# Performance work log

Hardware: AMD Instinct MI355X
Metric: run time of the kernel (lower is better)

Reference implementation:

```python
import jax, jax.numpy as jnp
from jax import lax
import numpy as np

NH = 8   # num_heads
WS = 7   # windowsize
SR = 2   # sr_ratio


def _conv(x, w, b, stride=1, padding=0, groups=1):
    y = lax.conv_general_dilated(x, w, (stride, stride), [(padding, padding)] * 2,
                                 dimension_numbers=('NCHW', 'OIHW', 'NCHW'),
                                 feature_group_count=groups)
    return y + b[None, :, None, None]


def _ln(x, g, b, eps=1e-5):
    m = x.mean(-1, keepdims=True)
    v = ((x - m) ** 2).mean(-1, keepdims=True)
    return (x - m) * lax.rsqrt(v + eps) * g + b


def _local_branch(q_, kv_img, dilation, stride, fc_w, sh_w, lc_w, lc_b, scale, H, W):
    # q_: [B,NH,N,hd]; kv_img: [B,C,H,W] with C = NH*hd
    B, C = kv_img.shape[0], kv_img.shape[1]
    hd = q_.shape[-1]
    pad_b = (-H) % stride
    pad_r = (-W) % stride
    kv = jnp.pad(kv_img, ((0, 0), (0, 0), (0, pad_b), (0, pad_r)), mode='reflect')
    nH, nW = (H + pad_b) // stride, (W + pad_r) // stride
    L = nH * nW
    # nn.Unfold(kernel=WS, stride, dilation): effective kernel == stride, so
    # windows tile exactly; sample each stride x stride tile at step `dilation`.
    kv = kv.reshape(B, C, nH, stride, nW, stride)[:, :, :, ::dilation, :, ::dilation]  # [B,C,nH,WS,nW,WS]
    kv = kv.transpose(0, 1, 3, 5, 2, 4).reshape(B, NH, hd, WS * WS, L)
    kv = kv.transpose(0, 1, 3, 4, 2).reshape(B, NH, WS * WS, L * hd)
    # AdaptiveAvgPool2d((None, hd)) on last dim of size L*hd -> hd buckets of L
    kv = kv.reshape(B, NH, WS * WS, hd, L).mean(-1)
    kv = (kv @ fc_w) @ sh_w                                  # [B,NH,49,2*hd]
    k_, v_ = kv[..., :hd], kv[..., hd:]
    attn = jax.nn.softmax(jnp.einsum('bhnd,bhkd->bhnk', q_, k_) * scale, axis=-1)
    v_img = v_.transpose(0, 1, 3, 2).reshape(B, C, WS, WS)
    v_ = v_ + _conv(v_img, lc_w, lc_b, padding=1, groups=C).reshape(B, NH, hd, WS * WS).transpose(0, 1, 3, 2)
    out = jnp.einsum('bhnk,bhkd->bhnd', attn, v_)            # [B,NH,N,hd]
    return out.transpose(0, 2, 1, 3).reshape(B, -1, C)


def setup_inputs() -> dict:
    key = jax.random.key(0)
    ks = jax.random.split(key, 24)
    B, H, W, dim = 2, 112, 112, 512
    N = H * W
    d0, d1, hd = 64, 224, 28
    dl = dim - d0  # 448

    def w(k, shape):
        return jax.random.normal(k, shape, jnp.float32) * 0.02

    return dict(
        x=jax.random.normal(ks[0], (B, N, dim), jnp.float32),
        Wq=w(ks[1], (dim, dim)),
        Wkv_g=w(ks[2], (d0, 2 * d0)),
        sr_w=w(ks[3], (d0, d0, SR, SR)), sr_b=w(ks[4], (d0,)),
        ln_g=jnp.ones((d0,), jnp.float32), ln_b=jnp.zeros((d0,), jnp.float32),
        lcg_w=w(ks[5], (d0, 1, 3, 3)), lcg_b=w(ks[6], (d0,)),
        kvl_dw=w(ks[7], (dl, 1, 3, 3)), kvl_db=w(ks[8], (dl,)),
        kvl_pw=w(ks[9], (dl, dl, 1, 1)), kvl_pb=w(ks[10], (dl,)),
        fc1_w=w(ks[11], (hd, hd)), sh1_w=w(ks[12], (hd, 2 * hd)),
        lc1_w=w(ks[13], (d1, 1, 3, 3)), lc1_b=w(ks[14], (d1,)),
        fc2_w=w(ks[15], (hd, hd)), sh2_w=w(ks[16], (hd, 2 * hd)),
        lc2_w=w(ks[17], (d1, 1, 3, 3)), lc2_b=w(ks[18], (d1,)),
        proj_w=w(ks[19], (dim, dim)), proj_b=w(ks[20], (dim,)),
        H=H, W=W,
    )


def reference(x, Wq, Wkv_g, sr_w, sr_b, ln_g, ln_b, lcg_w, lcg_b, kvl_dw, kvl_db,
              kvl_pw, kvl_pb, fc1_w, sh1_w, lc1_w, lc1_b, fc2_w, sh2_w, lc2_w, lc2_b,
              proj_w, proj_b, H, W):
    B, N, C = x.shape
    d0 = 64
    dl = C - d0        # 448
    hd = 224 // NH     # 28
    q = x @ Wq
    # ---- global spatially-reduced branch (1 head, dim 64) ----
    q_g = q[:, :, :d0]                                      # [B,N,64]
    x_g = x[:, :, :d0].transpose(0, 2, 1).reshape(B, d0, H, W)
    x_g = _conv(x_g, sr_w, sr_b, stride=SR)                 # [B,64,H/2,W/2]
    Hs, Ws_ = H // SR, W // SR
    Nr = Hs * Ws_
    x_g = _ln(x_g.reshape(B, d0, Nr).transpose(0, 2, 1), ln_g, ln_b)
    kvg = x_g @ Wkv_g
    k_g, v_g = kvg[..., :d0], kvg[..., d0:]
    attn_g = jax.nn.softmax(jnp.einsum('bnd,bmd->bnm', q_g, k_g) * d0 ** -0.5, axis=-1)
    v_img = v_g.transpose(0, 2, 1).reshape(B, d0, Hs, Ws_)
    v_g = v_g + _conv(v_img, lcg_w, lcg_b, padding=1, groups=d0).reshape(B, d0, Nr).transpose(0, 2, 1)
    out_g = jnp.einsum('bnm,bmd->bnd', attn_g, v_g)         # [B,N,64]
    # ---- local windowed branches (8 heads, dim 224 each) ----
    q_l = q[:, :, d0:].reshape(B, N, NH, -1).transpose(0, 2, 1, 3)  # [B,NH,N,56]
    x_l = x[:, :, d0:].reshape(B, H, W, dl).transpose(0, 3, 1, 2)
    kv_l = _conv(_conv(x_l, kvl_dw, kvl_db, padding=1, groups=dl), kvl_pw, kvl_pb)
    scale = hd ** -0.5
    out1 = _local_branch(q_l[:, :, :, :hd], kv_l[:, :224], 1, WS,
                         fc1_w, sh1_w, lc1_w, lc1_b, scale, H, W)
    out2 = _local_branch(q_l[:, :, :, hd:], kv_l[:, 224:], SR, SR * (WS - 1) + 1,
                         fc2_w, sh2_w, lc2_w, lc2_b, scale, H, W)
    return jnp.concatenate([out_g, out1, out2], -1) @ proj_w + proj_b
```

## Files before the change

kernel.cpp:

```cpp
#include <hip/hip_runtime.h>
#include <hip/hip_bf16.h>
#include <math.h>
#include <stdint.h>

static constexpr int B_    = 2;
static constexpr int N_    = 12544;
static constexpr int DIM_  = 512;
static constexpr int D0_   = 64;
static constexpr int DL_   = 448;
static constexpr int Himg  = 112;
static constexpr int Wimg  = 112;
static constexpr int HS_   = 56;
static constexpr int NR_   = 3136;
static constexpr int NH_   = 8;
static constexpr int HD_   = 28;
static constexpr int NSPLIT = 4;

typedef unsigned short ushort_t;
typedef __attribute__((ext_vector_type(8))) short short8_t;
typedef __attribute__((ext_vector_type(4))) float float4v;
typedef __attribute__((ext_vector_type(4))) unsigned uint4v;
typedef __attribute__((ext_vector_type(2))) unsigned uint2v;

static __device__ inline ushort_t bf16r(float x) {
    unsigned u = __builtin_bit_cast(unsigned, x);
    u = (u + 0x7FFFu + ((u >> 16) & 1u)) >> 16;
    return (ushort_t)u;
}
static __device__ inline float bf16tof(ushort_t h) {
    unsigned u = ((unsigned)h) << 16;
    return __builtin_bit_cast(float, u);
}
static __device__ inline unsigned pack_bf16(float lo, float hi) {
    unsigned a = __builtin_bit_cast(unsigned, lo);
    unsigned b = __builtin_bit_cast(unsigned, hi);
    a = (a + 0x7FFFu + ((a >> 16) & 1u)) >> 16;
    b = (b + 0x7FFFu + ((b >> 16) & 1u)) >> 16;
    return a | (b << 16);
}
static __device__ inline unsigned cvtpk(float lo, float hi) {
    float2 f2; f2.x = lo; f2.y = hi;
    __hip_bfloat162 h = __float22bfloat162_rn(f2);
    unsigned u;
    __builtin_memcpy(&u, &h, 4);
    return u;
}

using gptr_t = const __attribute__((address_space(1))) void*;
using lptr_t = __attribute__((address_space(3))) void*;
static __device__ inline void gload16(const void* g, void* l) {
    __builtin_amdgcn_global_load_lds((gptr_t)(uintptr_t)g, (lptr_t)(uintptr_t)l, 16, 0, 0);
}

template<bool HASBIAS, bool OUT16>
__global__ __launch_bounds__(256, 2)
void gemm_bf16_kernel(const ushort_t* __restrict__ A,
                      const ushort_t* __restrict__ Bt,
                      const float* __restrict__ bias,
                      void* __restrict__ Cv,
                      int Nn, int K, int ldc) {
    constexpr int BM = 128, BK = 64;
    __shared__ __align__(16) ushort_t As[BM * BK];
    __shared__ __align__(16) ushort_t Bs[BM * BK];
    const int bm = blockIdx.x * BM;
    const int bn = blockIdx.y * BM;
    const int tid = threadIdx.x;
    const int l15 = tid & 15;
    const int g   = (tid & 63) >> 4;
    const int w   = tid >> 6;
    const int wr  = w >> 1, wc = w & 1;

    float4v acc[4][4];
    #pragma unroll
    for (int m = 0; m < 4; ++m)
        #pragma unroll
        for (int n = 0; n < 4; ++n) acc[m][n] = (float4v){0.f, 0.f, 0.f, 0.f};

    for (int k0 = 0; k0 < K; k0 += BK) {
        #pragma unroll
        for (int i = 0; i < 4; ++i) {
            int c = i * 256 + tid;
            int r = c >> 3, ch = c & 7;
            int sch = ch ^ (r & 7);
            gload16(A  + (size_t)(bm + r) * K + k0 + sch * 8, (void*)(As + c * 8));
            gload16(Bt + (size_t)(bn + r) * K + k0 + sch * 8, (void*)(Bs + c * 8));
        }
        __syncthreads();

        short8_t af[4][2], bfr[4][2];
        #pragma unroll
        for (int m = 0; m < 4; ++m) {
            int ar = wr * 64 + m * 16 + l15;
            #pragma unroll
            for (int h = 0; h < 2; ++h)
                af[m][h] = *(const short8_t*)((const char*)As + ar * 128 + (((h * 4 + g) ^ (ar & 7)) * 16));
        }
        #pragma unroll
        for (int n = 0; n < 4; ++n) {
            int br = wc * 64 + n * 16 + l15;
            #pragma unroll
            for (int h = 0; h < 2; ++h)
                bfr[n][h] = *(const short8_t*)((const char*)Bs + br * 128 + (((h * 4 + g) ^ (br & 7)) * 16));
        }
        #pragma unroll
        for (int m = 0; m < 4; ++m)
            #pragma unroll
            for (int n = 0; n < 4; ++n) {
                acc[m][n] = __builtin_amdgcn_mfma_f32_16x16x32_bf16(af[m][0], bfr[n][0], acc[m][n], 0, 0, 0);
                acc[m][n] = __builtin_amdgcn_mfma_f32_16x16x32_bf16(af[m][1], bfr[n][1], acc[m][n], 0, 0, 0);
            }
        __syncthreads();
    }

    #pragma unroll
    for (int n = 0; n < 4; ++n) {
        int ccol = bn + wc * 64 + n * 16 + l15;
        if (ccol < Nn) {
            float bv = HASBIAS ? bias[ccol] : 0.f;
            #pragma unroll
            for (int m = 0; m < 4; ++m) {
                int crow = bm + wr * 64 + m * 16 + g * 4;
                #pragma unroll
                for (int j = 0; j < 4; ++j) {
                    float v = acc[m][n][j] + bv;
                    if (OUT16)
                        ((ushort_t*)Cv)[(size_t)(crow + j) * ldc + ccol] = bf16r(v);
                    else
                        ((float*)Cv)[(size_t)(crow + j) * ldc + ccol] = v;
                }
            }
        }
    }
}

__global__ __launch_bounds__(256)
void prep_kernel(const float* __restrict__ Wq, const float* __restrict__ kvl_pw,
                 const float* __restrict__ proj_w, const float* __restrict__ sr_w,
                 const float* __restrict__ x,
                 ushort_t* __restrict__ wqt, ushort_t* __restrict__ pwt,
                 ushort_t* __restrict__ projt, float* __restrict__ srwt,
                 ushort_t* __restrict__ xbf) {
    int idx = blockIdx.x * 256 + threadIdx.x;
    if (idx < 262144) {
        int n = idx >> 9, k = idx & 511;
        wqt[idx] = bf16r(Wq[(size_t)k * 512 + n]);
    } else if (idx < 491520) {
        int i = idx - 262144;
        int n = i / 448, k = i % 448;
        float v = (n < 448) ? kvl_pw[(size_t)n * 448 + k] : 0.f;
        pwt[i] = bf16r(v);
    } else if (idx < 753664) {
        int i = idx - 491520;
        int n = i >> 9, k = i & 511;
        projt[i] = bf16r(proj_w[(size_t)k * 512 + n]);
    } else if (idx < 770048) {
        int i = idx - 753664;
        int f = i >> 6, o2 = i & 63;
        srwt[i] = sr_w[o2 * 256 + f];
    } else {
        int i = idx - 770048;
        const float4v* p = (const float4v*)(x + (size_t)i * 8);
        float4v a = p[0], b = p[1];
        uint4v u;
        u[0] = pack_bf16(a[0], a[1]);
        u[1] = pack_bf16(a[2], a[3]);
        u[2] = pack_bf16(b[0], b[1]);
        u[3] = pack_bf16(b[2], b[3]);
        *(uint4v*)(xbf + (size_t)i * 8) = u;
    }
}

__global__ __launch_bounds__(256, 2)
void fused3_kernel(const ushort_t* __restrict__ xbf, const ushort_t* __restrict__ wqt,
                   ushort_t* __restrict__ q16,
                   const float* __restrict__ kvl_dw, const float* __restrict__ kvl_db,
                   ushort_t* __restrict__ dwtb,
                   const float* __restrict__ x, const float* __restrict__ srwt,
                   const float* __restrict__ sr_b, const float* __restrict__ ln_g,
                   const float* __restrict__ ln_b, const float* __restrict__ wkv,
                   ushort_t* __restrict__ kgb, float* __restrict__ vg) {
    const int bid = blockIdx.x;
    const int tid = threadIdx.x;
    __shared__ __align__(16) char smem[32768];

    if (bid < 784) {
        ushort_t* As = (ushort_t*)smem;
        ushort_t* Bs = (ushort_t*)(smem + 16384);
        const int bm = (bid % 196) * 128;
        const int bn = (bid / 196) * 128;
        const int l15 = tid & 15;
        const int g   = (tid & 63) >> 4;
        const int w   = tid >> 6;
        const int wr  = w >> 1, wc = w & 1;
        float4v acc[4][4];
        #pragma unroll
        for (int m = 0; m < 4; ++m)
            #pragma unroll
            for (int n = 0; n < 4; ++n) acc[m][n] = (float4v){0.f, 0.f, 0.f, 0.f};
        for (int k0 = 0; k0 < 512; k0 += 64) {
            #pragma unroll
            for (int i = 0; i < 4; ++i) {
                int c = i * 256 + tid;
                int r = c >> 3, ch = c & 7;
                int sch = ch ^ (r & 7);
                gload16(xbf + (size_t)(bm + r) * 512 + k0 + sch * 8, (void*)(As + c * 8));
                gload16(wqt + (size_t)(bn + r) * 512 + k0 + sch * 8, (void*)(Bs + c * 8));
            }
            __syncthreads();
            short8_t af[4][2], bfr[4][2];
            #pragma unroll
            for (int m = 0; m < 4; ++m) {
                int ar = wr * 64 + m * 16 + l15;
                #pragma unroll
                for (int h = 0; h < 2; ++h)
                    af[m][h] = *(const short8_t*)((const char*)As + ar * 128 + (((h * 4 + g) ^ (ar & 7)) * 16));
            }
            #pragma unroll
            for (int n = 0; n < 4; ++n) {
                int br = wc * 64 + n * 16 + l15;
                #pragma unroll
                for (int h = 0; h < 2; ++h)
                    bfr[n][h] = *(const short8_t*)((const char*)Bs + br * 128 + (((h * 4 + g) ^ (br & 7)) * 16));
            }
            #pragma unroll
            for (int m = 0; m < 4; ++m)
                #pragma unroll
                for (int n = 0; n < 4; ++n) {
                    acc[m][n] = __builtin_amdgcn_mfma_f32_16x16x32_bf16(af[m][0], bfr[n][0], acc[m][n], 0, 0, 0);
                    acc[m][n] = __builtin_amdgcn_mfma_f32_16x16x32_bf16(af[m][1], bfr[n][1], acc[m][n], 0, 0, 0);
                }
            __syncthreads();
        }
        #pragma unroll
        for (int n = 0; n < 4; ++n) {
            int ccol = bn + wc * 64 + n * 16 + l15;
            #pragma unroll
            for (int m = 0; m < 4; ++m) {
                int crow = bm + wr * 64 + m * 16 + g * 4;
                #pragma unroll
                for (int j = 0; j < 4; ++j)
                    q16[(size_t)(crow + j) * 512 + ccol] = bf16r(acc[m][n][j]);
            }
        }
    } else if (bid < 3528) {
        int idx = (bid - 784) * 256 + tid;
        int c4 = idx % 112;
        int t1 = idx / 112;
        int xx = t1 % 112;
        int t2 = t1 / 112;
        int yg = t2 % 28;
        int b  = t2 / 28;
        int c0 = c4 * 4;
        int y0 = yg * 4;
        float4v w4[9];
        #pragma unroll
        for (int kt = 0; kt < 9; ++kt) {
            w4[kt][0] = kvl_dw[(c0 + 0) * 9 + kt];
            w4[kt][1] = kvl_dw[(c0 + 1) * 9 + kt];
            w4[kt][2] = kvl_dw[(c0 + 2) * 9 + kt];
            w4[kt][3] = kvl_dw[(c0 + 3) * 9 + kt];
        }
        float4v bv = *(const float4v*)(kvl_db + c0);
        float4v acc[4];
        #pragma unroll
        for (int o2 = 0; o2 < 4; ++o2) acc[o2] = bv;
        #pragma unroll
        for (int yy = 0; yy < 6; ++yy) {
            int Y = y0 - 1 + yy;
            if (Y < 0 || Y >= Himg) continue;
            #pragma unroll
            for (int xt = 0; xt < 3; ++xt) {
                int X = xx - 1 + xt;
                if (X < 0 || X >= Wimg) continue;
                uint2v q2 = *(const uint2v*)(xbf + ((size_t)b * N_ + Y * Wimg + X) * DIM_ + D0_ + c0);
                float4v v;
                v[0] = bf16tof((ushort_t)(q2[0] & 0xffffu));
                v[1] = bf16tof((ushort_t)(q2[0] >> 16));
                v[2] = bf16tof((ushort_t)(q2[1] & 0xffffu));
                v[3] = bf16tof((ushort_t)(q2[1] >> 16));
                constexpr int olo_t[6] = {0, 0, 0, 1, 2, 3};
                constexpr int ohi_t[6] = {0, 1, 2, 3, 3, 3};
                #pragma unroll
                for (int o2 = olo_t[yy]; o2 <= ohi_t[yy]; ++o2) {
                    float4v wv = w4[(yy - o2) * 3 + xt];
                    acc[o2][0] += v[0] * wv[0];
                    acc[o2][1] += v[1] * wv[1];
                    acc[o2][2] += v[2] * wv[2];
                    acc[o2][3] += v[3] * wv[3];
                }
            }
        }
        #pragma unroll
        for (int o2 = 0; o2 < 4; ++o2) {
            uint2v pk;
            pk[0] = pack_bf16(acc[o2][0], acc[o2][1]);
            pk[1] = pack_bf16(acc[o2][2], acc[o2][3]);
            *(uint2v*)(dwtb + ((size_t)b * N_ + (y0 + o2) * Wimg + xx) * DL_ + c0) = pk;
        }
    } else {
        float* xs    = (float*)smem;
        float* lnv_s = (float*)(smem + 4096);
        const int blk4 = bid - 3528;
        const int grp  = tid >> 6;
        const int o    = tid & 63;
        const int pos  = blk4 * 4 + grp;
        const int b = pos / NR_, n = pos % NR_;
        const int y = n / HS_, xx = n % HS_;
        #pragma unroll
        for (int tap = 0; tap < 4; ++tap) {
            int ky = tap / 2, kx = tap % 2;
            xs[grp * 256 + tap * 64 + o] =
                x[((size_t)b * N_ + (2 * y + ky) * Wimg + 2 * xx + kx) * DIM_ + o];
        }
        __syncthreads();
        float sum = sr_b[o];
        for (int i = 0; i < 64; ++i) {
            const float* wr = srwt + (i * 4) * 64 + o;
            sum += xs[grp * 256 + 0 * 64 + i] * wr[0] + xs[grp * 256 + 1 * 64 + i] * wr[64]
                 + xs[grp * 256 + 2 * 64 + i] * wr[128] + xs[grp * 256 + 3 * 64 + i] * wr[192];
        }
        float m = sum;
        #pragma unroll
        for (int off = 1; off < 64; off <<= 1) m += __shfl_xor(m, off);
        m *= (1.0f / 64.0f);
        float d = sum - m;
        float v = d * d;
        #pragma unroll
        for (int off = 1; off < 64; off <<= 1) v += __shfl_xor(v, off);
        v *= (1.0f / 64.0f);
        float lnv = d * rsqrtf(v + 1e-5f) * ln_g[o] + ln_b[o];
        lnv_s[grp * 64 + o] = lnv;
        __syncthreads();
        float s0 = 0.f, s1 = 0.f;
        for (int i = 0; i < 64; ++i) {
            float lv = lnv_s[grp * 64 + i];
            s0 += lv * wkv[i * 128 + o];
            s1 += lv * wkv[i * 128 + o + 64];
        }
        const float SCK = 0.125f * 1.44269504088896340736f;
        kgb[((size_t)b * NR_ + n) * 64 + o] = bf16r(s0 * SCK);
        vg[((size_t)b * NR_ + n) * 64 + o] = s1;
    }
}

__global__ __launch_bounds__(256, 2)
void fused2_kernel(const ushort_t* __restrict__ dwtb, const ushort_t* __restrict__ pwt,
                   const float* __restrict__ kvl_pb, ushort_t* __restrict__ kvl16,
                   const float* __restrict__ vg, const float* __restrict__ lcg_w,
                   const float* __restrict__ lcg_b, ushort_t* __restrict__ vtb) {
    const int bid = blockIdx.x;
    const int tid = threadIdx.x;
    __shared__ __align__(16) char smem[32768];

    if (bid < 784) {
        ushort_t* As = (ushort_t*)smem;
        ushort_t* Bs = (ushort_t*)(smem + 16384);
        const int bm = (bid % 196) * 128;
        const int bn = (bid / 196) * 128;
        const int l15 = tid & 15;
        const int g   = (tid & 63) >> 4;
        const int w   = tid >> 6;
        const int wr  = w >> 1, wc = w & 1;
        float4v acc[4][4];
        #pragma unroll
        for (int m = 0; m < 4; ++m)
            #pragma unroll
            for (int n = 0; n < 4; ++n) acc[m][n] = (float4v){0.f, 0.f, 0.f, 0.f};
        for (int k0 = 0; k0 < 448; k0 += 64) {
            #pragma unroll
            for (int i = 0; i < 4; ++i) {
                int c = i * 256 + tid;
                int r = c >> 3, ch = c & 7;
                int sch = ch ^ (r & 7);
                gload16(dwtb + (size_t)(bm + r) * 448 + k0 + sch * 8, (void*)(As + c * 8));
                gload16(pwt  + (size_t)(bn + r) * 448 + k0 + sch * 8, (void*)(Bs + c * 8));
            }
            __syncthreads();
            short8_t af[4][2], bfr[4][2];
            #pragma unroll
            for (int m = 0; m < 4; ++m) {
                int ar = wr * 64 + m * 16 + l15;
                #pragma unroll
                for (int h = 0; h < 2; ++h)
                    af[m][h] = *(const short8_t*)((const char*)As + ar * 128 + (((h * 4 + g) ^ (ar & 7)) * 16));
            }
            #pragma unroll
            for (int n = 0; n < 4; ++n) {
                int br = wc * 64 + n * 16 + l15;
                #pragma unroll
                for (int h = 0; h < 2; ++h)
                    bfr[n][h] = *(const short8_t*)((const char*)Bs + br * 128 + (((h * 4 + g) ^ (br & 7)) * 16));
            }
            #pragma unroll
            for (int m = 0; m < 4; ++m)
                #pragma unroll
                for (int n = 0; n < 4; ++n) {
                    acc[m][n] = __builtin_amdgcn_mfma_f32_16x16x32_bf16(af[m][0], bfr[n][0], acc[m][n], 0, 0, 0);
                    acc[m][n] = __builtin_amdgcn_mfma_f32_16x16x32_bf16(af[m][1], bfr[n][1], acc[m][n], 0, 0, 0);
                }
            __syncthreads();
        }
        #pragma unroll
        for (int n = 0; n < 4; ++n) {
            int ccol = bn + wc * 64 + n * 16 + l15;
            if (ccol < 448) {
                float bv = kvl_pb[ccol];
                #pragma unroll
                for (int m = 0; m < 4; ++m) {
                    int crow = bm + wr * 64 + m * 16 + g * 4;
                    #pragma unroll
                    for (int j = 0; j < 4; ++j)
                        kvl16[(size_t)(crow + j) * 448 + ccol] = bf16r(acc[m][n][j] + bv);
                }
            }
        }
    } else {
        float* ld = (float*)smem;
        const int lb = bid - 784;
        const int b = lb / 49, n0 = (lb % 49) * 64;
        #pragma unroll
        for (int i = 0; i < 16; ++i) {
            int idx = i * 256 + tid;
            int n = idx >> 6, c = idx & 63;
            int nn = n0 + n;
            int y = nn / HS_, xx = nn % HS_;
            float sum = vg[((size_t)b * NR_ + nn) * 64 + c] + lcg_b[c];
            #pragma unroll
            for (int ky = 0; ky < 3; ++ky)
                #pragma unroll
                for (int kx = 0; kx < 3; ++kx) {
                    int yy = y + ky - 1, x2 = xx + kx - 1;
                    if (yy >= 0 && yy < HS_ && x2 >= 0 && x2 < HS_)
                        sum += vg[((size_t)b * NR_ + yy * HS_ + x2) * 64 + c] * lcg_w[c * 9 + ky * 3 + kx];
                }
            ld[n * 65 + c] = sum;
        }
        __syncthreads();
        #pragma unroll
        for (int i = 0; i < 16; ++i) {
            int idx = i * 256 + tid;
            int d = idx >> 6, nn = idx & 63;
            vtb[(size_t)(b * 64 + d) * NR_ + n0 + nn] = bf16r(ld[nn * 65 + d]);
        }
    }
}

template<int L, int NBW, int STRIDE, int DIL, int CHOFF>
__device__ inline void lm_body(int blk, int t, float* slo, float* shi,
                               const ushort_t* __restrict__ kvl16,
                               float* __restrict__ kvm) {
    const int n = blk % 49;
    const int h = (blk / 49) % NH_;
    const int b = blk / (49 * NH_);
    const int wy = n / 7, wx = n % 7;

    if (t < L) {
        const int by = t / NBW, bx = t % NBW;
        int Y = by * STRIDE + DIL * wy;
        int X = bx * STRIDE + DIL * wx;
        if (Y >= Himg) Y = 2 * Himg - 2 - Y;
        if (X >= Wimg) X = 2 * Wimg - 2 - X;
        const ushort_t* src = kvl16 + ((size_t)b * N_ + Y * Wimg + X) * DL_ + CHOFF + h * HD_;
        float v[28];
        #pragma unroll
        for (int i = 0; i < 7; ++i) {
            uint2v q2 = ((const uint2v*)src)[i];
            v[i * 4]     = bf16tof((ushort_t)(q2[0] & 0xffffu));
            v[i * 4 + 1] = bf16tof((ushort_t)(q2[0] >> 16));
            v[i * 4 + 2] = bf16tof((ushort_t)(q2[1] & 0xffffu));
            v[i * 4 + 3] = bf16tof((ushort_t)(q2[1] >> 16));
        }
        const int f0 = t * HD_;
        const int bin0 = f0 / L;
        const int nlo = min(HD_, (bin0 + 1) * L - f0);
        float s0 = 0.f, s1 = 0.f;
        #pragma unroll
        for (int j = 0; j < HD_; ++j) {
            if (j < nlo) s0 += v[j]; else s1 += v[j];
        }
        slo[t] = s0;
        shi[t] = s1;
    }
    __syncthreads();
    if (t < HD_) {
        const int t_lo = (t * L) / HD_;
        const int t_hi = min(L - 1, (t * L + L - 1) / HD_);
        float sum = 0.f;
        for (int u = t_lo; u <= t_hi; ++u) {
            int f0 = u * HD_;
            int b0 = f0 / L;
            int b1 = (f0 + HD_ - 1) / L;
            if (b0 == t) sum += slo[u];
            if (b1 == t && b1 != b0) sum += shi[u];
        }
        kvm[(size_t)blk * HD_ + t] = sum * (1.0f / (float)L);
    }
}

__global__ __launch_bounds__(512)
void fused_ag_lm_kernel(const ushort_t* __restrict__ q16,
                        const ushort_t* __restrict__ kgb,
                        const ushort_t* __restrict__ vtb,
                        ushort_t* __restrict__ osp16, float* __restrict__ mls,
                        const ushort_t* __restrict__ kvl16,
                        float* __restrict__ kvm1, float* __restrict__ kvm2) {
    const int bid = blockIdx.x;
    const int tid = threadIdx.x;
    __shared__ __align__(16) char smem[32768];
    ushort_t* Ks = (ushort_t*)smem;
    ushort_t* Vs = (ushort_t*)(smem + 16384);

    if (bid >= 784) {
        float* slo = (float*)smem;
        float* shi = (float*)(smem + 1024);
        int lmid = bid - 784;
        int blk = lmid % 784;
        if (lmid < 784) lm_body<256, 16, 7, 1, 0>(blk, tid, slo, shi, kvl16, kvm1);
        else            lm_body<81, 9, 13, 2, 224>(blk, tid, slo, shi, kvl16, kvm2);
        return;
    }

    const int split = (bid / 98) & 3;
    const int b     = (bid / 98) >> 2;
    const int q0    = (bid % 98) * 128;
    const int w     = tid >> 6;
    const int l     = tid & 63;
    const int l15   = l & 15;
    const int g     = l >> 4;
    const int lx    = l15 & 7;

    short8_t qf[2];
    {
        const ushort_t* qrow = q16 + ((size_t)b * N_ + q0 + w * 16 + l15) * DIM_;
        qf[0] = *(const short8_t*)(qrow + g * 8);
        qf[1] = *(const short8_t*)(qrow + g * 8 + 32);
    }

    float4v o[4];
    #pragma unroll
    for (int i = 0; i < 4; ++i) o[i] = (float4v){0.f, 0.f, 0.f, 0.f};
    float m_run = -3.0e38f, l_run = 0.f;

    const int stg_r   = tid >> 3;
    const int stg_sch = (tid & 7) ^ (stg_r & 7);
    const int stg_pr  = (stg_r & 32) | (((stg_r >> 2) & 3) << 3) | (((stg_r >> 4) & 1) << 2) | (stg_r & 3);
    auto stage = [&](int t, int buf) {
        const int k0 = t * 64;
        gload16(kgb + ((size_t)(b * NR_ + k0 + stg_pr) << 6) + stg_sch * 8,
                (void*)(Ks + buf * 4096 + tid * 8));
        gload16(vtb + (size_t)(b * 64 + stg_r) * NR_ + k0 + stg_sch * 8,
                (void*)(Vs + buf * 4096 + tid * 8));
    };

    auto compute = [&](const ushort_t* Kb, const ushort_t* Vb) {
        float4v sc[4];
        #pragma unroll
        for (int c = 0; c < 4; ++c) {
            float4v acc = (float4v){0.f, 0.f, 0.f, 0.f};
            #pragma unroll
            for (int dc = 0; dc < 2; ++dc) {
                int row = c * 16 + l15;
                short8_t ak = *(const short8_t*)((const char*)Kb + row * 128 + (((g + 4 * dc) ^ lx) * 16));
                acc = __builtin_amdgcn_mfma_f32_16x16x32_bf16(ak, qf[dc], acc, 0, 0, 0);
            }
            sc[c] = acc;
        }

        float tmax = fmaxf(fmaxf(fmaxf(sc[0][0], sc[0][1]), fmaxf(sc[0][2], sc[0][3])),
                           fmaxf(fmaxf(sc[1][0], sc[1][1]), fmaxf(sc[1][2], sc[1][3])));
        tmax = fmaxf(tmax, fmaxf(fmaxf(fmaxf(sc[2][0], sc[2][1]), fmaxf(sc[2][2], sc[2][3])),
                                 fmaxf(fmaxf(sc[3][0], sc[3][1]), fmaxf(sc[3][2], sc[3][3]))));

        if (__any(tmax > m_run + 11.0f)) {
            float rmax = fmaxf(tmax, __shfl_xor(tmax, 16));
            rmax = fmaxf(rmax, __shfl_xor(rmax, 32));
            float m_new = fmaxf(m_run, rmax);
            float corr = __builtin_amdgcn_exp2f(m_run - m_new);
            float co[4];
            #pragma unroll
            for (int r = 0; r < 4; ++r) co[r] = __shfl(corr, g * 4 + r);
            #pragma unroll
            for (int dc = 0; dc < 4; ++dc)
                #pragma unroll
                for (int r = 0; r < 4; ++r) o[dc][r] *= co[r];
            l_run *= corr;
            m_run = m_new;
        }

        float p[4][4];
        float ladd = 0.f;
        #pragma unroll
        for (int c = 0; c < 4; ++c)
            #pragma unroll
            for (int r = 0; r < 4; ++r) {
                float pe = __builtin_amdgcn_exp2f(sc[c][r] - m_run);
                p[c][r] = pe;
                ladd += pe;
            }
        l_run += ladd;

        #pragma unroll
        for (int kkc = 0; kkc < 2; ++kkc) {
            uint4v au;
            au[0] = cvtpk(p[2 * kkc][0],     p[2 * kkc][1]);
            au[1] = cvtpk(p[2 * kkc][2],     p[2 * kkc][3]);
            au[2] = cvtpk(p[2 * kkc + 1][0], p[2 * kkc + 1][1]);
            au[3] = cvtpk(p[2 * kkc + 1][2], p[2 * kkc + 1][3]);
            short8_t ap = __builtin_bit_cast(short8_t, au);
            #pragma unroll
            for (int dc = 0; dc < 4; ++dc) {
                int vrow = dc * 16 + l15;
                short8_t bv = *(const short8_t*)((const char*)Vb + vrow * 128 + (((kkc * 4 + g) ^ lx) * 16));
                o[dc] = __builtin_amdgcn_mfma_f32_16x16x32_bf16(ap, bv, o[dc], 0, 0, 0);
            }
        }
    };

    const int t0 = (split * 49) / 4;
    const int t1 = ((split + 1) * 49) / 4;
    int t = t0;
    for (; t + 1 < t1; t += 2) {
        stage(t, 0);
        stage(t + 1, 1);
        __syncthreads();
        compute(Ks, Vs);
        compute(Ks + 4096, Vs + 4096);
        __syncthreads();
    }
    if (t < t1) {
        stage(t, 0);
        __syncthreads();
        compute(Ks, Vs);
    }

    float l_tot = l_run;
    l_tot += __shfl_xor(l_tot, 16);
    l_tot += __shfl_xor(l_tot, 32);

    const size_t rbase = (size_t)(split * B_ + b) * N_;
    #pragma unroll
    for (int dc = 0; dc < 4; ++dc)
        #pragma unroll
        for (int r = 0; r < 4; ++r) {
            int row = q0 + w * 16 + g * 4 + r;
            osp16[(rbase + row) * 64 + dc * 16 + l15] = bf16r(o[dc][r]);
        }
    if (l < 16) {
        int row = q0 + w * 16 + l15;
        mls[(rbase + row) * 2]     = m_run;
        mls[(rbase + row) * 2 + 1] = l_tot;
    }
}

__global__ __launch_bounds__(256)
void fcsh_vconv_kernel(const float* __restrict__ kvm1, const float* __restrict__ fc1w,
                       const float* __restrict__ sh1w, float* __restrict__ kv1,
                       const float* __restrict__ kvm2, const float* __restrict__ fc2w,
                       const float* __restrict__ sh2w, float* __restrict__ kv2,
                       const float* __restrict__ lc1w, const float* __restrict__ lc1b,
                       float* __restrict__ v1c,
                       const float* __restrict__ lc2w, const float* __restrict__ lc2b,
                       float* __restrict__ v2c) {
    int bh2 = blockIdx.x;
    const int branch = (bh2 >= 16);
    const float* kvm = branch ? kvm2 : kvm1;
    const float* fcw = branch ? fc2w : fc1w;
    const float* shw = branch ? sh2w : sh1w;
    const float* lcw = branch ? lc2w : lc1w;
    const float* lcb = branch ? lc2b : lc1b;
    float* kvout     = branch ? kv2 : kv1;
    float* vcout     = branch ? v2c : v1c;
    int bh = branch ? bh2 - 16 : bh2;
    const int h = bh % NH_;
    __shared__ float kin[49][28];
    __shared__ float tmp[49][28];
    __shared__ float fw[28 * 28];
    __shared__ float sw[28 * 56];
    __shared__ float outs[49][56];
    int t = threadIdx.x;
    for (int i = t; i < 49 * 28; i += 256) kin[i / 28][i % 28] = kvm[bh * 49 * 28 + i];
    for (int i = t; i < 28 * 28; i += 256) fw[i] = fcw[i];
    for (int i = t; i < 28 * 56; i += 256) sw[i] = shw[i];
    __syncthreads();
    for (int i = t; i < 49 * 28; i += 256) {
        int rr = i / 28, j = i % 28;
        float s = 0.f;
        for (int k = 0; k < 28; ++k) s += kin[rr][k] * fw[k * 28 + j];
        tmp[rr][j] = s;
    }
    __syncthreads();
    for (int i = t; i < 49 * 56; i += 256) {
        int rr = i / 56, j = i % 56;
        float s = 0.f;
        for (int k = 0; k < 28; ++k) s += tmp[rr][k] * sw[k * 56 + j];
        outs[rr][j] = s;
        kvout[bh * 49 * 56 + i] = s;
    }
    __syncthreads();
    for (int i = t; i < 49 * 28; i += 256) {
        int d = i % 28, n = i / 28;
        int y = n / 7, xx = n % 7;
        int c = h * HD_ + d;
        float sum = outs[n][28 + d] + lcb[c];
        #pragma unroll
        for (int ky = 0; ky < 3; ++ky)
            #pragma unroll
            for (int kx = 0; kx < 3; ++kx) {
                int yy = y + ky - 1, x2 = xx + kx - 1;
                if (yy >= 0 && yy < 7 && x2 >= 0 && x2 < 7)
                    sum += outs[yy * 7 + x2][28 + d] * lcw[c * 9 + ky * 3 + kx];
            }
        vcout[bh * 49 * 28 + i] = sum;
    }
}

__global__ __launch_bounds__(256)
void fused_local_comb_kernel(const ushort_t* __restrict__ q16,
                             const float* __restrict__ kv1, const float* __restrict__ v1c,
                             const float* __restrict__ kv2, const float* __restrict__ v2c,
                             const ushort_t* __restrict__ osp16, const float* __restrict__ mls,
                             ushort_t* __restrict__ catb) {
    const int bid = blockIdx.x;
    const int tid = threadIdx.x;
    __shared__ __align__(16) ushort_t Ks[64 * 32];
    __shared__ __align__(16) ushort_t Vt[32 * 64];

    if (bid >= 6272) {
        int idx = (bid - 6272) * 256 + tid;
        int col = idx & 63;
        size_t rn = (size_t)(idx >> 6);
        const size_t BN = (size_t)B_ * N_;
        float ms[NSPLIT], ls[NSPLIT];
        float m = -3.0e38f;
        #pragma unroll
        for (int s = 0; s < NSPLIT; ++s) {
            ms[s] = mls[(s * BN + rn) * 2];
            ls[s] = mls[(s * BN + rn) * 2 + 1];
            m = fmaxf(m, ms[s]);
        }
        float lsum = 0.f, acc = 0.f;
        #pragma unroll
        for (int s = 0; s < NSPLIT; ++s) {
            float wgt = __builtin_amdgcn_exp2f(ms[s] - m);
            lsum += ls[s] * wgt;
            acc  += bf16tof(osp16[(s * BN + rn) * 64 + col]) * wgt;
        }
        catb[rn * DIM_ + col] = bf16r(acc / lsum);
        return;
    }

    const int ybh    = bid / 196;
    const int branch = ybh & 1;
    const int bh     = ybh >> 1;
    const int b      = bh >> 3, h = bh & 7;
    const int q0     = (bid % 196) * 64;
    const int w      = tid >> 6;
    const int l      = tid & 63;
    const int l15    = l & 15;
    const int g      = l >> 4;
    const float SC2K = 0.1889822365046136f * 1.44269504088896340736f;

    const float* kvsh = branch ? kv2 : kv1;
    const float* vc   = branch ? v2c : v1c;
    const int qoff    = D0_ + h * 56 + branch * 28;
    const int outoff  = (branch ? D0_ + 224 : D0_) + h * HD_;

    {
        int row = tid >> 2, lc = tid & 3;
        int pr = (row & 32) | (((row >> 2) & 3) << 3) | (((row >> 4) & 1) << 2) | (row & 3);
        uint4v u = (uint4v){0u, 0u, 0u, 0u};
        if (pr < 49) {
            const float* src = kvsh + (bh * 49 + pr) * 56 + lc * 8;
            float vv[8];
            #pragma unroll
            for (int j2 = 0; j2 < 8; ++j2)
                vv[j2] = (lc * 8 + j2 < 28) ? src[j2] * SC2K : 0.f;
            u[0] = cvtpk(vv[0], vv[1]);
            u[1] = cvtpk(vv[2], vv[3]);
            u[2] = cvtpk(vv[4], vv[5]);
            u[3] = cvtpk(vv[6], vv[7]);
        }
        *(uint4v*)(Ks + row * 32 + (lc ^ (row & 3)) * 8) = u;
    }
    {
        int row = tid >> 3, lc = tid & 7;
        uint4v u = (uint4v){0u, 0u, 0u, 0u};
        if (row < 28) {
            float vv[8];
            #pragma unroll
            for (int j2 = 0; j2 < 8; ++j2) {
                int kc = lc * 8 + j2;
                vv[j2] = (kc < 49) ? vc[(bh * 49 + kc) * 28 + row] : 0.f;
            }
            u[0] = cvtpk(vv[0], vv[1]);
            u[1] = cvtpk(vv[2], vv[3]);
            u[2] = cvtpk(vv[4], vv[5]);
            u[3] = cvtpk(vv[6], vv[7]);
        }
        *(uint4v*)(Vt + row * 64 + (lc ^ (row & 7)) * 8) = u;
    }
    short8_t qf;
    {
        const ushort_t* qp = q16 + ((size_t)b * N_ + q0 + w * 16 + l15) * DIM_ + qoff + g * 8;
        uint2v a01 = *(const uint2v*)qp;
        uint2v a23 = (g < 3) ? *(const uint2v*)(qp + 4) : (uint2v){0u, 0u};
        uint4v uv;
        uv[0] = a01[0]; uv[1] = a01[1]; uv[2] = a23[0]; uv[3] = a23[1];
        qf = __builtin_bit_cast(short8_t, uv);
    }
    __syncthreads();

    float4v sc4[4];
    #pragma unroll
    for (int c = 0; c < 4; ++c) {
        int row = c * 16 + l15;
        short8_t ak = *(const short8_t*)(Ks + row * 32 + ((g ^ (row & 3)) * 8));
        float4v acc = (float4v){0.f, 0.f, 0.f, 0.f};
        sc4[c] = __builtin_amdgcn_mfma_f32_16x16x32_bf16(ak, qf, acc, 0, 0, 0);
    }

    float tmax = fmaxf(fmaxf(fmaxf(sc4[0][0], sc4[0][1]), fmaxf(sc4[0][2], sc4[0][3])),
                       fmaxf(fmaxf(sc4[1][0], sc4[1][1]), fmaxf(sc4[1][2], sc4[1][3])));
    tmax = fmaxf(tmax, fmaxf(fmaxf(fmaxf(sc4[2][0], sc4[2][1]), fmaxf(sc4[2][2], sc4[2][3])),
                             fmaxf(fmaxf(sc4[3][0], sc4[3][1]), fmaxf(sc4[3][2], sc4[3][3]))));
    tmax = fmaxf(tmax, __shfl_xor(tmax, 16));
    tmax = fmaxf(tmax, __shfl_xor(tmax, 32));

    float p[4][4];
    float lsum = 0.f;
    #pragma unroll
    for (int c = 0; c < 4; ++c)
        #pragma unroll
        for (int r = 0; r < 4; ++r) {
            float pe = __builtin_amdgcn_exp2f(sc4[c][r] - tmax);
            if (c >= 2 && (8 * g + 4 * (c & 1) + r) >= 17) pe = 0.f;
            p[c][r] = pe;
            lsum += pe;
        }
    lsum += __shfl_xor(lsum, 16);
    lsum += __shfl_xor(lsum, 32);
    float inv = 1.0f / lsum;

    float4v o2[2];
    o2[0] = (float4v){0.f, 0.f, 0.f, 0.f};
    o2[1] = (float4v){0.f, 0.f, 0.f, 0.f};
    #pragma unroll
    for (int kkc = 0; kkc < 2; ++kkc) {
        uint4v au;
        au[0] = cvtpk(p[2 * kkc][0],     p[2 * kkc][1]);
        au[1] = cvtpk(p[2 * kkc][2],     p[2 * kkc][3]);
        au[2] = cvtpk(p[2 * kkc + 1][0], p[2 * kkc + 1][1]);
        au[3] = cvtpk(p[2 * kkc + 1][2], p[2 * kkc + 1][3]);
        short8_t ap = __builtin_bit_cast(short8_t, au);
        #pragma unroll
        for (int dc = 0; dc < 2; ++dc) {
            int vrow = dc * 16 + l15;
            short8_t bv = *(const short8_t*)(Vt + vrow * 64 + (((kkc * 4 + g) ^ (vrow & 7)) * 8));
            o2[dc] = __builtin_amdgcn_mfma_f32_16x16x32_bf16(ap, bv, o2[dc], 0, 0, 0);
        }
    }

    float irow[4];
    #pragma unroll
    for (int r = 0; r < 4; ++r) irow[r] = __shfl(inv, g * 4 + r);
    #pragma unroll
    for (int dc = 0; dc < 2; ++dc) {
        int d = dc * 16 + l15;
        if (d < 28) {
            #pragma unroll
            for (int r = 0; r < 4; ++r) {
                int row = q0 + w * 16 + g * 4 + r;
                catb[((size_t)b * N_ + row) * DIM_ + outoff + d] = bf16r(o2[dc][r] * irow[r]);
            }
        }
    }
}

extern "C" void kernel_launch(void* const* d_in, const int* in_sizes, int n_in,
                              void* d_out, int out_size, void* d_ws, size_t ws_size,
                              hipStream_t stream) {
    const float* x      = (const float*)d_in[0];
    const float* Wq     = (const float*)d_in[1];
    const float* Wkv_g  = (const float*)d_in[2];
    const float* sr_w   = (const float*)d_in[3];
    const float* sr_b   = (const float*)d_in[4];
    const float* ln_g   = (const float*)d_in[5];
    const float* ln_b   = (const float*)d_in[6];
    const float* lcg_w  = (const float*)d_in[7];
    const float* lcg_b  = (const float*)d_in[8];
    const float* kvl_dw = (const float*)d_in[9];
    const float* kvl_db = (const float*)d_in[10];
    const float* kvl_pw = (const float*)d_in[11];
    const float* kvl_pb = (const float*)d_in[12];
    const float* fc1_w  = (const float*)d_in[13];
    const float* sh1_w  = (const float*)d_in[14];
    const float* lc1_w  = (const float*)d_in[15];
    const float* lc1_b  = (const float*)d_in[16];
    const float* fc2_w  = (const float*)d_in[17];
    const float* sh2_w  = (const float*)d_in[18];
    const float* lc2_w  = (const float*)d_in[19];
    const float* lc2_b  = (const float*)d_in[20];
    const float* proj_w = (const float*)d_in[21];
    const float* proj_b = (const float*)d_in[22];
    float* out = (float*)d_out;
    char* base = (char*)d_ws;

    size_t o = 0;
    auto alloc = [&](size_t bytes) -> void* {
        void* p = base + o;
        o = (o + bytes + 255) & ~(size_t)255;
        return p;
    };
    ushort_t* q16   = (ushort_t*)alloc((size_t)B_ * N_ * DIM_ * 2);
    ushort_t* kvl16 = (ushort_t*)alloc((size_t)B_ * N_ * DL_ * 2);
    ushort_t* osp16 = (ushort_t*)alloc((size_t)NSPLIT * B_ * N_ * 64 * 2);
    float*    mls   = (float*)   alloc((size_t)NSPLIT * B_ * N_ * 2 * 4);
    ushort_t* xcat  = (ushort_t*)alloc((size_t)B_ * N_ * DIM_ * 2);
    ushort_t* dwtb  = (ushort_t*)alloc((size_t)B_ * N_ * DL_ * 2);
    ushort_t* kgb   = (ushort_t*)alloc((size_t)B_ * NR_ * 64 * 2);
    float*    vg    = (float*)   alloc((size_t)B_ * NR_ * 64 * 4);
    ushort_t* vtb   = (ushort_t*)alloc((size_t)B_ * 64 * NR_ * 2);
    ushort_t* wqt   = (ushort_t*)alloc((size_t)512 * 512 * 2);
    ushort_t* pwt   = (ushort_t*)alloc((size_t)512 * 448 * 2);
    ushort_t* projt = (ushort_t*)alloc((size_t)512 * 512 * 2);
    float*    srwt  = (float*)   alloc((size_t)256 * 64 * 4);
    float*    kvm1  = (float*)   alloc((size_t)B_ * NH_ * 49 * HD_ * 4);
    float*    kvm2  = (float*)   alloc((size_t)B_ * NH_ * 49 * HD_ * 4);
    float*    kv1   = (float*)   alloc((size_t)B_ * NH_ * 49 * 56 * 4);
    float*    kv2   = (float*)   alloc((size_t)B_ * NH_ * 49 * 56 * 4);
    float*    v1c   = (float*)   alloc((size_t)B_ * NH_ * 49 * HD_ * 4);
    float*    v2c   = (float*)   alloc((size_t)B_ * NH_ * 49 * HD_ * 4);
    ushort_t* xbf   = xcat;
    ushort_t* catb  = xcat;

    const int M = B_ * N_;

    prep_kernel<<<9280, 256, 0, stream>>>(Wq, kvl_pw, proj_w, sr_w, x,
                                          wqt, pwt, projt, srwt, xbf);

    fused3_kernel<<<5096, 256, 0, stream>>>(xbf, wqt, q16,
                                            kvl_dw, kvl_db, dwtb,
                                            x, srwt, sr_b, ln_g, ln_b, Wkv_g,
                                            kgb, vg);

    fused2_kernel<<<882, 256, 0, stream>>>(dwtb, pwt, kvl_pb, kvl16,
                                           vg, lcg_w, lcg_b, vtb);

    fused_ag_lm_kernel<<<2352, 512, 0, stream>>>(q16, kgb, vtb, osp16, mls,
                                                 kvl16, kvm1, kvm2);

    fcsh_vconv_kernel<<<32, 256, 0, stream>>>(kvm1, fc1_w, sh1_w, kv1,
                                              kvm2, fc2_w, sh2_w, kv2,
                                              lc1_w, lc1_b, v1c,
                                              lc2_w, lc2_b, v2c);

    fused_local_comb_kernel<<<12544, 256, 0, stream>>>(q16, kv1, v1c, kv2, v2c,
                                                       osp16, mls, catb);

    gemm_bf16_kernel<true, false><<<dim3(M / 128, 4), 256, 0, stream>>>(
        catb, projt, proj_b, out, 512, 512, 512);
}
```

Before: 250.4 us.

## Move depthwise conv into prep kernel and merge both GEMMs into one launch

The depthwise 3x3 conv now runs inside the prep kernel and reads fp32 x directly instead of the bf16 copy. That lets the pointwise GEMM (dwtb x pwt) run in the same launch as the Q GEMM and the sr/LN/kv blocks, with one shared block-dispatch path. The local-conv and transpose of vg moves to its own small kernel. The goal is to rebalance work across launches and put the two large GEMMs in one grid for better occupancy. In exchange, the depthwise conv now sits in the bandwidth-bound prep kernel, and it reads fp32 x, which doubles the bytes loaded for that step.

```diff
diff --git a/kernel.cpp b/kernel.cpp
--- a/kernel.cpp
+++ b/kernel.cpp
@@ -137,9 +137,10 @@
 void prep_kernel(const float* __restrict__ Wq, const float* __restrict__ kvl_pw,
                  const float* __restrict__ proj_w, const float* __restrict__ sr_w,
                  const float* __restrict__ x,
+                 const float* __restrict__ kvl_dw, const float* __restrict__ kvl_db,
                  ushort_t* __restrict__ wqt, ushort_t* __restrict__ pwt,
                  ushort_t* __restrict__ projt, float* __restrict__ srwt,
-                 ushort_t* __restrict__ xbf) {
+                 ushort_t* __restrict__ xbf, ushort_t* __restrict__ dwtb) {
     int idx = blockIdx.x * 256 + threadIdx.x;
     if (idx < 262144) {
         int n = idx >> 9, k = idx & 511;
@@ -157,7 +158,7 @@
         int i = idx - 753664;
         int f = i >> 6, o2 = i & 63;
         srwt[i] = sr_w[o2 * 256 + f];
-    } else {
+    } else if (idx < 2375680) {
         int i = idx - 770048;
         const float4v* p = (const float4v*)(x + (size_t)i * 8);
         float4v a = p[0], b = p[1];
@@ -167,85 +168,10 @@
         u[2] = pack_bf16(b[0], b[1]);
         u[3] = pack_bf16(b[2], b[3]);
         *(uint4v*)(xbf + (size_t)i * 8) = u;
-    }
-}
-
-__global__ __launch_bounds__(256, 2)
-void fused3_kernel(const ushort_t* __restrict__ xbf, const ushort_t* __restrict__ wqt,
-                   ushort_t* __restrict__ q16,
-                   const float* __restrict__ kvl_dw, const float* __restrict__ kvl_db,
-                   ushort_t* __restrict__ dwtb,
-                   const float* __restrict__ x, const float* __restrict__ srwt,
-                   const float* __restrict__ sr_b, const float* __restrict__ ln_g,
-                   const float* __restrict__ ln_b, const float* __restrict__ wkv,
-                   ushort_t* __restrict__ kgb, float* __restrict__ vg) {
-    const int bid = blockIdx.x;
-    const int tid = threadIdx.x;
-    __shared__ __align__(16) char smem[32768];
-
-    if (bid < 784) {
-        ushort_t* As = (ushort_t*)smem;
-        ushort_t* Bs = (ushort_t*)(smem + 16384);
-        const int bm = (bid % 196) * 128;
-        const int bn = (bid / 196) * 128;
-        const int l15 = tid & 15;
-        const int g   = (tid & 63) >> 4;
-        const int w   = tid >> 6;
-        const int wr  = w >> 1, wc = w & 1;
-        float4v acc[4][4];
-        #pragma unroll
-        for (int m = 0; m < 4; ++m)
-            #pragma unroll
-            for (int n = 0; n < 4; ++n) acc[m][n] = (float4v){0.f, 0.f, 0.f, 0.f};
-        for (int k0 = 0; k0 < 512; k0 += 64) {
-            #pragma unroll
-            for (int i = 0; i < 4; ++i) {
-                int c = i * 256 + tid;
-                int r = c >> 3, ch = c & 7;
-                int sch = ch ^ (r & 7);
-                gload16(xbf + (size_t)(bm + r) * 512 + k0 + sch * 8, (void*)(As + c * 8));
-                gload16(wqt + (size_t)(bn + r) * 512 + k0 + sch * 8, (void*)(Bs + c * 8));
-            }
-            __syncthreads();
-            short8_t af[4][2], bfr[4][2];
-            #pragma unroll
-            for (int m = 0; m < 4; ++m) {
-                int ar = wr * 64 + m * 16 + l15;
-                #pragma unroll
-                for (int h = 0; h < 2; ++h)
-                    af[m][h] = *(const short8_t*)((const char*)As + ar * 128 + (((h * 4 + g) ^ (ar & 7)) * 16));
-            }
-            #pragma unroll
-            for (int n = 0; n < 4; ++n) {
-                int br = wc * 64 + n * 16 + l15;
-                #pragma unroll
-                for (int h = 0; h < 2; ++h)
-                    bfr[n][h] = *(const short8_t*)((const char*)Bs + br * 128 + (((h * 4 + g) ^ (br & 7)) * 16));
-            }
-            #pragma unroll
-            for (int m = 0; m < 4; ++m)
-                #pragma unroll
-                for (int n = 0; n < 4; ++n) {
-                    acc[m][n] = __builtin_amdgcn_mfma_f32_16x16x32_bf16(af[m][0], bfr[n][0], acc[m][n], 0, 0, 0);
-                    acc[m][n] = __builtin_amdgcn_mfma_f32_16x16x32_bf16(af[m][1], bfr[n][1], acc[m][n], 0, 0, 0);
-                }
-            __syncthreads();
-        }
-        #pragma unroll
-        for (int n = 0; n < 4; ++n) {
-            int ccol = bn + wc * 64 + n * 16 + l15;
-            #pragma unroll
-            for (int m = 0; m < 4; ++m) {
-                int crow = bm + wr * 64 + m * 16 + g * 4;
-                #pragma unroll
-                for (int j = 0; j < 4; ++j)
-                    q16[(size_t)(crow + j) * 512 + ccol] = bf16r(acc[m][n][j]);
-            }
-        }
-    } else if (bid < 3528) {
-        int idx = (bid - 784) * 256 + tid;
-        int c4 = idx % 112;
-        int t1 = idx / 112;
+    } else {
+        int i = idx - 2375680;
+        int c4 = i % 112;
+        int t1 = i / 112;
         int xx = t1 % 112;
         int t2 = t1 / 112;
         int yg = t2 % 28;
@@ -272,12 +198,7 @@
             for (int xt = 0; xt < 3; ++xt) {
                 int X = xx - 1 + xt;
                 if (X < 0 || X >= Wimg) continue;
-                uint2v q2 = *(const uint2v*)(xbf + ((size_t)b * N_ + Y * Wimg + X) * DIM_ + D0_ + c0);
-                float4v v;
-                v[0] = bf16tof((ushort_t)(q2[0] & 0xffffu));
-                v[1] = bf16tof((ushort_t)(q2[0] >> 16));
-                v[2] = bf16tof((ushort_t)(q2[1] & 0xffffu));
-                v[3] = bf16tof((ushort_t)(q2[1] >> 16));
+                float4v v = *(const float4v*)(x + ((size_t)b * N_ + Y * Wimg + X) * DIM_ + D0_ + c0);
                 constexpr int olo_t[6] = {0, 0, 0, 1, 2, 3};
                 constexpr int ohi_t[6] = {0, 1, 2, 3, 3, 3};
                 #pragma unroll
@@ -297,10 +218,107 @@
             pk[1] = pack_bf16(acc[o2][2], acc[o2][3]);
             *(uint2v*)(dwtb + ((size_t)b * N_ + (y0 + o2) * Wimg + xx) * DL_ + c0) = pk;
         }
+    }
+}
+
+__global__ __launch_bounds__(256, 2)
+void fused3_kernel(const ushort_t* __restrict__ xbf, const ushort_t* __restrict__ wqt,
+                   ushort_t* __restrict__ q16,
+                   const ushort_t* __restrict__ dwtb, const ushort_t* __restrict__ pwt,
+                   const float* __restrict__ kvl_pb, ushort_t* __restrict__ kvl16,
+                   const float* __restrict__ x, const float* __restrict__ srwt,
+                   const float* __restrict__ sr_b, const float* __restrict__ ln_g,
+                   const float* __restrict__ ln_b, const float* __restrict__ wkv,
+                   ushort_t* __restrict__ kgb, float* __restrict__ vg) {
+    const int bid = blockIdx.x;
+    const int tid = threadIdx.x;
+    __shared__ __align__(16) char smem[32768];
+
+    if (bid < 1568) {
+        ushort_t* As = (ushort_t*)smem;
+        ushort_t* Bs = (ushort_t*)(smem + 16384);
+        const bool isQ = (bid < 784);
+        const int lb  = isQ ? bid : bid - 784;
+        const int K   = isQ ? 512 : 448;
+        const ushort_t* A  = isQ ? xbf : dwtb;
+        const ushort_t* Bt = isQ ? wqt : pwt;
+        const int bm = (lb % 196) * 128;
+        const int bn = (lb / 196) * 128;
+        const int l15 = tid & 15;
+        const int g   = (tid & 63) >> 4;
+        const int w   = tid >> 6;
+        const int wr  = w >> 1, wc = w & 1;
+        float4v acc[4][4];
+        #pragma unroll
+        for (int m = 0; m < 4; ++m)
+            #pragma unroll
+            for (int n = 0; n < 4; ++n) acc[m][n] = (float4v){0.f, 0.f, 0.f, 0.f};
+        for (int k0 = 0; k0 < K; k0 += 64) {
+            #pragma unroll
+            for (int i = 0; i < 4; ++i) {
+                int c = i * 256 + tid;
+                int r = c >> 3, ch = c & 7;
+                int sch = ch ^ (r & 7);
+                gload16(A  + (size_t)(bm + r) * K + k0 + sch * 8, (void*)(As + c * 8));
+                gload16(Bt + (size_t)(bn + r) * K + k0 + sch * 8, (void*)(Bs + c * 8));
+            }
+            __syncthreads();
+            short8_t af[4][2], bfr[4][2];
+            #pragma unroll
+            for (int m = 0; m < 4; ++m) {
+                int ar = wr * 64 + m * 16 + l15;
+                #pragma unroll
+                for (int h = 0; h < 2; ++h)
+                    af[m][h] = *(const short8_t*)((const char*)As + ar * 128 + (((h * 4 + g) ^ (ar & 7)) * 16));
+            }
+            #pragma unroll
+            for (int n = 0; n < 4; ++n) {
+                int br = wc * 64 + n * 16 + l15;
+                #pragma unroll
+                for (int h = 0; h < 2; ++h)
+                    bfr[n][h] = *(const short8_t*)((const char*)Bs + br * 128 + (((h * 4 + g) ^ (br & 7)) * 16));
+            }
+            #pragma unroll
+            for (int m = 0; m < 4; ++m)
+                #pragma unroll
+                for (int n = 0; n < 4; ++n) {
+                    acc[m][n] = __builtin_amdgcn_mfma_f32_16x16x32_bf16(af[m][0], bfr[n][0], acc[m][n], 0, 0, 0);
+                    acc[m][n] = __builtin_amdgcn_mfma_f32_16x16x32_bf16(af[m][1], bfr[n][1], acc[m][n], 0, 0, 0);
+                }
+            __syncthreads();
+        }
+        if (isQ) {
+            #pragma unroll
+            for (int n = 0; n < 4; ++n) {
+                int ccol = bn + wc * 64 + n * 16 + l15;
+                #pragma unroll
+                for (int m = 0; m < 4; ++m) {
+                    int crow = bm + wr * 64 + m * 16 + g * 4;
+                    #pragma unroll
+                    for (int j = 0; j < 4; ++j)
+                        q16[(size_t)(crow + j) * 512 + ccol] = bf16r(acc[m][n][j]);
+                }
+            }
+        } else {
+            #pragma unroll
+            for (int n = 0; n < 4; ++n) {
+                int ccol = bn + wc * 64 + n * 16 + l15;
+                if (ccol < 448) {
+                    float bv = kvl_pb[ccol];
+                    #pragma unroll
+                    for (int m = 0; m < 4; ++m) {
+                        int crow = bm + wr * 64 + m * 16 + g * 4;
+                        #pragma unroll
+                        for (int j = 0; j < 4; ++j)
+                            kvl16[(size_t)(crow + j) * 448 + ccol] = bf16r(acc[m][n][j] + bv);
+                    }
+                }
+            }
+        }
     } else {
         float* xs    = (float*)smem;
         float* lnv_s = (float*)(smem + 4096);
-        const int blk4 = bid - 3528;
+        const int blk4 = bid - 1568;
         const int grp  = tid >> 6;
         const int o    = tid & 63;
         const int pos  = blk4 * 4 + grp;
@@ -343,105 +361,34 @@
     }
 }
 
-__global__ __launch_bounds__(256, 2)
-void fused2_kernel(const ushort_t* __restrict__ dwtb, const ushort_t* __restrict__ pwt,
-                   const float* __restrict__ kvl_pb, ushort_t* __restrict__ kvl16,
-                   const float* __restrict__ vg, const float* __restrict__ lcg_w,
-                   const float* __restrict__ lcg_b, ushort_t* __restrict__ vtb) {
-    const int bid = blockIdx.x;
-    const int tid = threadIdx.x;
-    __shared__ __align__(16) char smem[32768];
-
-    if (bid < 784) {
-        ushort_t* As = (ushort_t*)smem;
-        ushort_t* Bs = (ushort_t*)(smem + 16384);
-        const int bm = (bid % 196) * 128;
-        const int bn = (bid / 196) * 128;
-        const int l15 = tid & 15;
-        const int g   = (tid & 63) >> 4;
-        const int w   = tid >> 6;
-        const int wr  = w >> 1, wc = w & 1;
-        float4v acc[4][4];
-        #pragma unroll
-        for (int m = 0; m < 4; ++m)
-            #pragma unroll
-            for (int n = 0; n < 4; ++n) acc[m][n] = (float4v){0.f, 0.f, 0.f, 0.f};
-        for (int k0 = 0; k0 < 448; k0 += 64) {
-            #pragma unroll
-            for (int i = 0; i < 4; ++i) {
-                int c = i * 256 + tid;
-                int r = c >> 3, ch = c & 7;
-                int sch = ch ^ (r & 7);
-                gload16(dwtb + (size_t)(bm + r) * 448 + k0 + sch * 8, (void*)(As + c * 8));
-                gload16(pwt  + (size_t)(bn + r) * 448 + k0 + sch * 8, (void*)(Bs + c * 8));
-            }
-            __syncthreads();
-            short8_t af[4][2], bfr[4][2];
-            #pragma unroll
-            for (int m = 0; m < 4; ++m) {
-                int ar = wr * 64 + m * 16 + l15;
-                #pragma unroll
-                for (int h = 0; h < 2; ++h)
-                    af[m][h] = *(const short8_t*)((const char*)As + ar * 128 + (((h * 4 + g) ^ (ar & 7)) * 16));
-            }
-            #pragma unroll
-            for (int n = 0; n < 4; ++n) {
-                int br = wc * 64 + n * 16 + l15;
-                #pragma unroll
-                for (int h = 0; h < 2; ++h)
-                    bfr[n][h] = *(const short8_t*)((const char*)Bs + br * 128 + (((h * 4 + g) ^ (br & 7)) * 16));
-            }
-            #pragma unroll
-            for (int m = 0; m < 4; ++m)
-                #pragma unroll
-                for (int n = 0; n < 4; ++n) {
-                    acc[m][n] = __builtin_amdgcn_mfma_f32_16x16x32_bf16(af[m][0], bfr[n][0], acc[m][n], 0, 0, 0);
-                    acc[m][n] = __builtin_amdgcn_mfma_f32_16x16x32_bf16(af[m][1], bfr[n][1], acc[m][n], 0, 0, 0);
-                }
-            __syncthreads();
-        }
-        #pragma unroll
-        for (int n = 0; n < 4; ++n) {
-            int ccol = bn + wc * 64 + n * 16 + l15;
-            if (ccol < 448) {
-                float bv = kvl_pb[ccol];
-                #pragma unroll
-                for (int m = 0; m < 4; ++m) {
-                    int crow = bm + wr * 64 + m * 16 + g * 4;
-                    #pragma unroll
-                    for (int j = 0; j < 4; ++j)
-                        kvl16[(size_t)(crow + j) * 448 + ccol] = bf16r(acc[m][n][j] + bv);
-                }
-            }
-        }
-    } else {
-        float* ld = (float*)smem;
-        const int lb = bid - 784;
-        const int b = lb / 49, n0 = (lb % 49) * 64;
-        #pragma unroll
-        for (int i = 0; i < 16; ++i) {
-            int idx = i * 256 + tid;
-            int n = idx >> 6, c = idx & 63;
-            int nn = n0 + n;
-            int y = nn / HS_, xx = nn % HS_;
-            float sum = vg[((size_t)b * NR_ + nn) * 64 + c] + lcg_b[c];
-            #pragma unroll
-            for (int ky = 0; ky < 3; ++ky)
-                #pragma unroll
-                for (int kx = 0; kx < 3; ++kx) {
-                    int yy = y + ky - 1, x2 = xx + kx - 1;
-                    if (yy >= 0 && yy < HS_ && x2 >= 0 && x2 < HS_)
-                        sum += vg[((size_t)b * NR_ + yy * HS_ + x2) * 64 + c] * lcg_w[c * 9 + ky * 3 + kx];
-                }
-            ld[n * 65 + c] = sum;
-        }
-        __syncthreads();
-        #pragma unroll
-        for (int i = 0; i < 16; ++i) {
-            int idx = i * 256 + tid;
-            int d = idx >> 6, nn = idx & 63;
-            vtb[(size_t)(b * 64 + d) * NR_ + n0 + nn] = bf16r(ld[nn * 65 + d]);
-        }
+__global__ __launch_bounds__(256)
+void lcgvt_kernel(const float* __restrict__ vg, const float* __restrict__ w,
+                  const float* __restrict__ bias, ushort_t* __restrict__ vtb) {
+    __shared__ float ld[64][65];
+    const int b = blockIdx.y, n0 = blockIdx.x * 64, tid = threadIdx.x;
+    #pragma unroll
+    for (int i = 0; i < 16; ++i) {
+        int idx = i * 256 + tid;
+        int n = idx >> 6, c = idx & 63;
+        int nn = n0 + n;
+        int y = nn / HS_, xx = nn % HS_;
+        float sum = vg[((size_t)b * NR_ + nn) * 64 + c] + bias[c];
+        #pragma unroll
+        for (int ky = 0; ky < 3; ++ky)
+            #pragma unroll
+            for (int kx = 0; kx < 3; ++kx) {
+                int yy = y + ky - 1, x2 = xx + kx - 1;
+                if (yy >= 0 && yy < HS_ && x2 >= 0 && x2 < HS_)
+                    sum += vg[((size_t)b * NR_ + yy * HS_ + x2) * 64 + c] * w[c * 9 + ky * 3 + kx];
+            }
+        ld[n][c] = sum;
+    }
+    __syncthreads();
+    #pragma unroll
+    for (int i = 0; i < 16; ++i) {
+        int idx = i * 256 + tid;
+        int d = idx >> 6, nn = idx & 63;
+        vtb[(size_t)(b * 64 + d) * NR_ + n0 + nn] = bf16r(ld[nn][d]);
     }
 }
 
@@ -935,16 +882,16 @@
 
     const int M = B_ * N_;
 
-    prep_kernel<<<9280, 256, 0, stream>>>(Wq, kvl_pw, proj_w, sr_w, x,
-                                          wqt, pwt, projt, srwt, xbf);
-
-    fused3_kernel<<<5096, 256, 0, stream>>>(xbf, wqt, q16,
-                                            kvl_dw, kvl_db, dwtb,
+    prep_kernel<<<12024, 256, 0, stream>>>(Wq, kvl_pw, proj_w, sr_w, x,
+                                           kvl_dw, kvl_db,
+                                           wqt, pwt, projt, srwt, xbf, dwtb);
+
+    fused3_kernel<<<3136, 256, 0, stream>>>(xbf, wqt, q16,
+                                            dwtb, pwt, kvl_pb, kvl16,
                                             x, srwt, sr_b, ln_g, ln_b, Wkv_g,
                                             kgb, vg);
 
-    fused2_kernel<<<882, 256, 0, stream>>>(dwtb, pwt, kvl_pb, kvl16,
-                                           vg, lcg_w, lcg_b, vtb);
+    lcgvt_kernel<<<dim3(NR_ / 64, B_), 256, 0, stream>>>(vg, lcg_w, lcg_b, vtb);
 
     fused_ag_lm_kernel<<<2352, 512, 0, stream>>>(q16, kgb, vtb, osp16, mls,
                                                  kvl16, kvm1, kvm2);
```

Result: no change. 251.6 us (+0.5%).
